# Kernel tuning notes

Hardware: AMD Instinct MI355X
Metric: run time of the kernel (lower is better)

The kernel has to match this reference:

```python
import jax, jax.numpy as jnp
import numpy as np

N = 50000      # nodes
E = 800000     # edges
IN, HID, OUT = 256, 64, 64
H1, H2 = 4, 1
NEG_SLOPE = 0.2  # DGL GATConv default


def gat_layer(x, W, a_l, a_r, b, src, dst, n_heads, d_out, activation=None):
    # x: [N, F_in]; W: [F_in, n_heads*d_out]; a_l/a_r: [n_heads, d_out]; b: [n_heads*d_out]
    z = (x @ W).reshape(N, n_heads, d_out)                      # [N,H,D]
    el = jnp.sum(z * a_l[None], axis=-1)                        # [N,H] score from src side
    er = jnp.sum(z * a_r[None], axis=-1)                        # [N,H] score from dst side
    e = jax.nn.leaky_relu(el[src] + er[dst], NEG_SLOPE)         # [E,H]
    # edge-softmax normalized over incoming edges of each dst node
    m = jax.ops.segment_max(e, dst, num_segments=N)             # [N,H]
    ex = jnp.exp(e - m[dst])                                    # [E,H]
    s = jax.ops.segment_sum(ex, dst, num_segments=N)            # [N,H]
    alpha = ex / s[dst]                                         # [E,H]
    # scatter-weighted aggregation of neighbor (src) features
    msg = alpha[:, :, None] * z[src]                            # [E,H,D]
    out = jax.ops.segment_sum(msg, dst, num_segments=N)         # [N,H,D]
    out = out + b.reshape(1, n_heads, d_out)
    if activation is not None:
        out = activation(out)
    return out


def setup_inputs() -> dict:
    key = jax.random.key(0)
    ks = jax.random.split(key, 12)
    x = jax.random.normal(ks[0], (N, IN), dtype=jnp.float32)
    src = jax.random.randint(ks[1], (E,), 0, N, dtype=jnp.int32)
    dst = jax.random.randint(ks[2], (E,), 0, N, dtype=jnp.int32)
    sc1 = 1.0 / np.sqrt(IN)
    sc2 = 1.0 / np.sqrt(HID * H1)
    W1 = jax.random.normal(ks[3], (IN, H1 * HID), dtype=jnp.float32) * sc1
    al1 = jax.random.normal(ks[4], (H1, HID), dtype=jnp.float32) * 0.1
    ar1 = jax.random.normal(ks[5], (H1, HID), dtype=jnp.float32) * 0.1
    b1 = jnp.zeros((H1 * HID,), dtype=jnp.float32)
    W2 = jax.random.normal(ks[6], (HID * H1, H2 * OUT), dtype=jnp.float32) * sc2
    al2 = jax.random.normal(ks[7], (H2, OUT), dtype=jnp.float32) * 0.1
    ar2 = jax.random.normal(ks[8], (H2, OUT), dtype=jnp.float32) * 0.1
    b2 = jnp.zeros((H2 * OUT,), dtype=jnp.float32)
    return {"x": x, "W1": W1, "al1": al1, "ar1": ar1, "b1": b1,
            "W2": W2, "al2": al2, "ar2": ar2, "b2": b2,
            "src": src, "dst": dst}


def reference(x, W1, al1, ar1, b1, W2, al2, ar2, b2, src, dst):
    # layer 1: GATConv(IN -> HID, H1 heads), elu activation, then flatten heads
    h = gat_layer(x, W1, al1, ar1, b1, src, dst, H1, HID, activation=jax.nn.elu)
    h = h.reshape(N, H1 * HID)
    # layer 2: GATConv(HID*H1 -> OUT, H2 heads), no activation, mean over heads
    h = gat_layer(h, W2, al2, ar2, b2, src, dst, H2, OUT, activation=None)
    return h.mean(axis=1)  # [N, OUT]
```

## Files before the change

kernel.cpp:

```cpp
#include <hip/hip_runtime.h>
#include <hip/hip_bf16.h>
#include <math.h>

#define NN 50000
#define EE 800000
#define FIN 256
#define HID 64
#define OUTD 64
#define H1 4
#define H2 1

typedef __attribute__((ext_vector_type(8))) short short8;
typedef __attribute__((ext_vector_type(4))) short short4v;
typedef __attribute__((ext_vector_type(4))) float f32x4;


__device__ __forceinline__ unsigned short f2bf(float f) {
    unsigned u = __float_as_uint(f);
    unsigned r = (u + 0x7FFFu + ((u >> 16) & 1u)) >> 16;
    return (unsigned short)r;
}
__device__ __forceinline__ float bf2f(unsigned short u) {
    return __uint_as_float(((unsigned)u) << 16);
}


__global__ void hist_kernel(const int* __restrict__ dst, int* __restrict__ deg, int nE) {
    int e = blockIdx.x * 256 + threadIdx.x;
    if (e < nE) atomicAdd(&deg[dst[e]], 1);
}

__global__ void scan_block(const int* __restrict__ in, int* __restrict__ out,
                           int* __restrict__ bsums, int n) {
    __shared__ int sh[256];
    int i = blockIdx.x * 256 + threadIdx.x;
    int v = (i < n) ? in[i] : 0;
    sh[threadIdx.x] = v;
    __syncthreads();
    for (int off = 1; off < 256; off <<= 1) {
        int t = 0;
        if (threadIdx.x >= off) t = sh[threadIdx.x - off];
        __syncthreads();
        if (threadIdx.x >= off) sh[threadIdx.x] += t;
        __syncthreads();
    }
    if (i < n) out[i] = sh[threadIdx.x] - v;
    if (threadIdx.x == 255) bsums[blockIdx.x] = sh[255];
}

__global__ void scan_bsums(int* __restrict__ bsums, int nb) {
    __shared__ int sh[256];
    int v = (threadIdx.x < nb) ? bsums[threadIdx.x] : 0;
    sh[threadIdx.x] = v;
    __syncthreads();
    for (int off = 1; off < 256; off <<= 1) {
        int t = 0;
        if (threadIdx.x >= off) t = sh[threadIdx.x - off];
        __syncthreads();
        if (threadIdx.x >= off) sh[threadIdx.x] += t;
        __syncthreads();
    }
    if (threadIdx.x < nb) bsums[threadIdx.x] = sh[threadIdx.x] - v;
}

__global__ void add_offsets(int* __restrict__ out, const int* __restrict__ bsums,
                            int n, int Etot) {
    int i = blockIdx.x * 256 + threadIdx.x;
    if (i < n) out[i] += bsums[blockIdx.x];
    if (i == 0) out[n] = Etot;
}

__global__ void fill_csr(const int* __restrict__ src, const int* __restrict__ dst,
                         const int* __restrict__ rowptr, int* __restrict__ fillc,
                         int* __restrict__ csr_src, int nE) {
    int e = blockIdx.x * 256 + threadIdx.x;
    if (e < nE) {
        int d = dst[e];
        int pos = rowptr[d] + atomicAdd(&fillc[d], 1);
        csr_src[pos] = src[e];
    }
}


__global__ void wsplit(const float* __restrict__ W1, const float* __restrict__ W2,
                       short* __restrict__ W1th, short* __restrict__ W1tl,
                       short* __restrict__ W2th, short* __restrict__ W2tl) {
    int n = blockIdx.x;
    int k = threadIdx.x;
    if (n < 256) {
        float v = W1[(size_t)k * 256 + n];
        unsigned short hi = f2bf(v);
        unsigned short lo = f2bf(v - bf2f(hi));
        W1th[n * 256 + k] = (short)hi;
        W1tl[n * 256 + k] = (short)lo;
    } else {
        int n2 = n - 256;
        float v = W2[(size_t)k * 64 + n2];
        unsigned short hi = f2bf(v);
        unsigned short lo = f2bf(v - bf2f(hi));
        W2th[n2 * 256 + k] = (short)hi;
        W2tl[n2 * 256 + k] = (short)lo;
    }
}


template<int MF, int WR, int WC, int NT, int H, bool ASPLIT>
__global__ __launch_bounds__(256) void gemm_bf16x2(
    const void* __restrict__ Av, const short* __restrict__ Bth, const short* __restrict__ Btl,
    const float* __restrict__ al, const float* __restrict__ ar,
    unsigned short* __restrict__ zb, float* __restrict__ el, float* __restrict__ er,
    int M, int K)
{
    constexpr int BM = WR * MF * 16;
    constexpr int BN = WC * 64;
    __shared__ short Ah[128 * 40];
    __shared__ short Al[ASPLIT ? 128 * 40 : 8];
    __shared__ short Bh[BN * 40], Bl[BN * 40];

    const int bm = blockIdx.x * BM;
    const int bn = blockIdx.y * BN;
    const int t = threadIdx.x;
    const int wid = t >> 6;
    const int lane = t & 63;
    const int lr = lane & 15;
    const int lg = lane >> 4;
    const int wr = wid / WC;
    const int wc = wid % WC;

    f32x4 acc[MF][4];
#pragma unroll
    for (int mf = 0; mf < MF; ++mf)
#pragma unroll
        for (int nf = 0; nf < 4; ++nf) acc[mf][nf] = (f32x4)(0.f);

    for (int k0 = 0; k0 < K; k0 += 32) {
        if constexpr (ASPLIT) {
            const float* A = (const float*)Av;
#pragma unroll
            for (int q = 0; q < 4; ++q) {
                int linear = q * 256 + t;
                int row = linear >> 3;
                int kq = (linear & 7) * 4;
                int grow = bm + row;
                float4 av = make_float4(0.f, 0.f, 0.f, 0.f);
                if (grow < M) av = *(const float4*)(A + (size_t)grow * K + k0 + kq);
                short4v hi, lo;
                unsigned short h0 = f2bf(av.x); hi.x = (short)h0; lo.x = (short)f2bf(av.x - bf2f(h0));
                unsigned short h1v = f2bf(av.y); hi.y = (short)h1v; lo.y = (short)f2bf(av.y - bf2f(h1v));
                unsigned short h2v = f2bf(av.z); hi.z = (short)h2v; lo.z = (short)f2bf(av.z - bf2f(h2v));
                unsigned short h3v = f2bf(av.w); hi.w = (short)h3v; lo.w = (short)f2bf(av.w - bf2f(h3v));
                *(short4v*)&Ah[row * 40 + kq] = hi;
                *(short4v*)&Al[row * 40 + kq] = lo;
            }
        } else {
            const unsigned short* A = (const unsigned short*)Av;
#pragma unroll
            for (int q = 0; q < 2; ++q) {
                int linear = q * 256 + t;
                int row = linear >> 2;
                int k8 = (linear & 3) * 8;
                int grow = bm + row;
                short8 v = (short8)(0);
                if (grow < M) v = *(const short8*)(A + (size_t)grow * K + k0 + k8);
                *(short8*)&Ah[row * 40 + k8] = v;
            }
        }
#pragma unroll
        for (int q = 0; q < BN / 64; ++q) {
            int linear = q * 256 + t;
            int n = linear >> 2;
            int k8 = (linear & 3) * 8;
            short8 vh = *(const short8*)(Bth + (size_t)(bn + n) * K + k0 + k8);
            short8 vl = *(const short8*)(Btl + (size_t)(bn + n) * K + k0 + k8);
            *(short8*)&Bh[n * 40 + k8] = vh;
            *(short8*)&Bl[n * 40 + k8] = vl;
        }
        __syncthreads();

        short8 ah[MF], alo[MF], bh[4], blo[4];
#pragma unroll
        for (int mf = 0; mf < MF; ++mf) {
            int row = wr * MF * 16 + mf * 16 + lr;
            ah[mf] = *(const short8*)&Ah[row * 40 + lg * 8];
            if constexpr (ASPLIT) alo[mf] = *(const short8*)&Al[row * 40 + lg * 8];
        }
#pragma unroll
        for (int nf = 0; nf < 4; ++nf) {
            int col = wc * 64 + nf * 16 + lr;
            bh[nf]  = *(const short8*)&Bh[col * 40 + lg * 8];
            blo[nf] = *(const short8*)&Bl[col * 40 + lg * 8];
        }
#pragma unroll
        for (int mf = 0; mf < MF; ++mf)
#pragma unroll
            for (int nf = 0; nf < 4; ++nf) {
                acc[mf][nf] = __builtin_amdgcn_mfma_f32_16x16x32_bf16(ah[mf], bh[nf],  acc[mf][nf], 0, 0, 0);
                acc[mf][nf] = __builtin_amdgcn_mfma_f32_16x16x32_bf16(ah[mf], blo[nf], acc[mf][nf], 0, 0, 0);
                if constexpr (ASPLIT)
                    acc[mf][nf] = __builtin_amdgcn_mfma_f32_16x16x32_bf16(alo[mf], bh[nf], acc[mf][nf], 0, 0, 0);
            }
        __syncthreads();
    }

    const int h = (bn + wc * 64) >> 6;
    float alv[4], arv[4];
#pragma unroll
    for (int nf = 0; nf < 4; ++nf) {
        alv[nf] = al[h * 64 + nf * 16 + lr];
        arv[nf] = ar[h * 64 + nf * 16 + lr];
    }
#pragma unroll
    for (int mf = 0; mf < MF; ++mf) {
#pragma unroll
        for (int j = 0; j < 4; ++j) {
            int row = bm + wr * MF * 16 + mf * 16 + lg * 4 + j;
            float sel = 0.f, ser = 0.f;
#pragma unroll
            for (int nf = 0; nf < 4; ++nf) {
                float v = acc[mf][nf][j];
                sel += v * alv[nf];
                ser += v * arv[nf];
                if (row < M)
                    zb[(size_t)row * NT + bn + wc * 64 + nf * 16 + lr] = f2bf(v);
            }
#pragma unroll
            for (int off = 1; off <= 8; off <<= 1) {
                sel += __shfl_xor(sel, off);
                ser += __shfl_xor(ser, off);
            }
            if (lr == 0 && row < M) {
                el[(size_t)row * H + h] = sel;
                er[(size_t)row * H + h] = ser;
            }
        }
    }
}


__global__ __launch_bounds__(256) void gat_aggregate_h4(
    const unsigned short* __restrict__ zb,
    const float* __restrict__ el,
    const float* __restrict__ er,
    const int* __restrict__ rowptr, const int* __restrict__ csr_src,
    const float* __restrict__ bias,
    unsigned short* __restrict__ out,
    int Nn)
{
    __shared__ float p_lds[4][64][4];
    __shared__ int   s_lds[4][64];
    int wid = threadIdx.x >> 6;
    int lane = threadIdx.x & 63;
    int n = blockIdx.x * 4 + wid;
    if (n >= Nn) return;
    int start = rowptr[n], end = rowptr[n + 1];
    int deg = end - start;
    float4 er4 = *(const float4*)(er + (size_t)n * 4);
    int hsel = lane >> 4;

    float4 acc = make_float4(0.f, 0.f, 0.f, 0.f);
    float4 ssum = make_float4(0.f, 0.f, 0.f, 0.f);
    float m = -INFINITY;

    for (int c0 = 0; c0 < deg; c0 += 64) {
        int nc = min(64, deg - c0);
        int s_l = 0;
        float4 e4 = make_float4(-INFINITY, -INFINITY, -INFINITY, -INFINITY);
        float emax_l = -INFINITY;
        if (lane < nc) {
            s_l = csr_src[start + c0 + lane];
            float4 el4 = *(const float4*)(el + (size_t)s_l * 4);
            e4.x = el4.x + er4.x; e4.x = e4.x > 0.f ? e4.x : 0.2f * e4.x;
            e4.y = el4.y + er4.y; e4.y = e4.y > 0.f ? e4.y : 0.2f * e4.y;
            e4.z = el4.z + er4.z; e4.z = e4.z > 0.f ? e4.z : 0.2f * e4.z;
            e4.w = el4.w + er4.w; e4.w = e4.w > 0.f ? e4.w : 0.2f * e4.w;
            emax_l = fmaxf(fmaxf(e4.x, e4.y), fmaxf(e4.z, e4.w));
        }
        float cm = emax_l;
#pragma unroll
        for (int off = 32; off; off >>= 1) cm = fmaxf(cm, __shfl_xor(cm, off));
        float newm = fmaxf(m, cm);
        float scale = __expf(m - newm);
        ssum.x *= scale; ssum.y *= scale; ssum.z *= scale; ssum.w *= scale;
        acc.x *= scale;  acc.y *= scale;  acc.z *= scale;  acc.w *= scale;
        m = newm;
        float4 p4 = make_float4(0.f, 0.f, 0.f, 0.f);
        if (lane < nc) {
            p4.x = __expf(e4.x - m);
            p4.y = __expf(e4.y - m);
            p4.z = __expf(e4.z - m);
            p4.w = __expf(e4.w - m);
        }
        float4 cs = p4;
#pragma unroll
        for (int off = 32; off; off >>= 1) {
            cs.x += __shfl_xor(cs.x, off);
            cs.y += __shfl_xor(cs.y, off);
            cs.z += __shfl_xor(cs.z, off);
            cs.w += __shfl_xor(cs.w, off);
        }
        ssum.x += cs.x; ssum.y += cs.y; ssum.z += cs.z; ssum.w += cs.w;
        *(float4*)&p_lds[wid][lane][0] = p4;
        s_lds[wid][lane] = s_l;

        const unsigned short* zlane = zb + lane * 4;
        for (int tt = 0; tt < nc; tt += 8) {
            float w[8]; int sv[8];
#pragma unroll
            for (int j = 0; j < 8; ++j) {
                int idx = tt + j;
                int ic = idx < nc ? idx : 0;
                w[j] = idx < nc ? p_lds[wid][ic][hsel] : 0.f;
                sv[j] = s_lds[wid][ic];
            }
            ushort4 u[8];
#pragma unroll
            for (int j = 0; j < 8; ++j)
                u[j] = *(const ushort4*)(zlane + (size_t)sv[j] * 256);
#pragma unroll
            for (int j = 0; j < 8; ++j) {
                acc.x = fmaf(w[j], bf2f(u[j].x), acc.x);
                acc.y = fmaf(w[j], bf2f(u[j].y), acc.y);
                acc.z = fmaf(w[j], bf2f(u[j].z), acc.z);
                acc.w = fmaf(w[j], bf2f(u[j].w), acc.w);
            }
        }
    }
    float s_h = hsel == 0 ? ssum.x : hsel == 1 ? ssum.y : hsel == 2 ? ssum.z : ssum.w;
    float inv = s_h > 0.f ? 1.f / s_h : 0.f;
    float4 b4 = *(const float4*)(bias + lane * 4);
    float ox = acc.x * inv + b4.x; ox = ox > 0.f ? ox : expm1f(ox);
    float oy = acc.y * inv + b4.y; oy = oy > 0.f ? oy : expm1f(oy);
    float oz = acc.z * inv + b4.z; oz = oz > 0.f ? oz : expm1f(oz);
    float ow = acc.w * inv + b4.w; ow = ow > 0.f ? ow : expm1f(ow);
    ushort4 o;
    o.x = f2bf(ox); o.y = f2bf(oy); o.z = f2bf(oz); o.w = f2bf(ow);
    *(ushort4*)(out + (size_t)n * 256 + lane * 4) = o;
}


__global__ void gat_aggregate_bf(const unsigned short* __restrict__ zb,
                                 const float* __restrict__ el, const float* __restrict__ er,
                                 const int* __restrict__ rowptr, const int* __restrict__ csr_src,
                                 const float* __restrict__ bias,
                                 float* __restrict__ out, int Nn)
{
    int gw = (blockIdx.x * blockDim.x + threadIdx.x) >> 6;
    int lane = threadIdx.x & 63;
    int n = gw;
    if (n >= Nn) return;
    int start = rowptr[n], end = rowptr[n + 1];
    int deg = end - start;
    float ern = er[n];

    int group = lane >> 4;
    int gl = lane & 15;

    float4 acc = make_float4(0.f, 0.f, 0.f, 0.f);
    float m = -INFINITY;
    float ssum = 0.f;

    for (int c0 = 0; c0 < deg; c0 += 64) {
        int nc = min(64, deg - c0);
        int s_l = 0;
        float e_l = -INFINITY;
        if (lane < nc) {
            s_l = csr_src[start + c0 + lane];
            float e = el[s_l] + ern;
            e_l = e > 0.f ? e : 0.2f * e;
        }
        float cm = e_l;
#pragma unroll
        for (int off = 32; off; off >>= 1) cm = fmaxf(cm, __shfl_xor(cm, off));
        float newm = fmaxf(m, cm);
        float scale = __expf(m - newm);
        ssum *= scale;
        acc.x *= scale; acc.y *= scale; acc.z *= scale; acc.w *= scale;
        m = newm;
        float p_l = (lane < nc) ? __expf(e_l - m) : 0.f;
        float cs = p_l;
#pragma unroll
        for (int off = 32; off; off >>= 1) cs += __shfl_xor(cs, off);
        ssum += cs;

        int nIter = (nc + 3) >> 2;
        for (int i0 = 0; i0 < nIter; i0 += 4) {
            float w[4]; int sv[4];
#pragma unroll
            for (int j = 0; j < 4; ++j) {
                int tt = group + 4 * (i0 + j);
                int tc = tt & 63;
                float wv = __shfl(p_l, tc);
                int s = __shfl(s_l, tc);
                w[j] = (tt < nc) ? wv : 0.f;
                sv[j] = s;
            }
            ushort4 u[4];
#pragma unroll
            for (int j = 0; j < 4; ++j)
                u[j] = *(const ushort4*)(zb + (size_t)sv[j] * 64 + gl * 4);
#pragma unroll
            for (int j = 0; j < 4; ++j) {
                acc.x = fmaf(w[j], bf2f(u[j].x), acc.x);
                acc.y = fmaf(w[j], bf2f(u[j].y), acc.y);
                acc.z = fmaf(w[j], bf2f(u[j].z), acc.z);
                acc.w = fmaf(w[j], bf2f(u[j].w), acc.w);
            }
        }
    }
#pragma unroll
    for (int off = 16; off <= 32; off <<= 1) {
        acc.x += __shfl_xor(acc.x, off);
        acc.y += __shfl_xor(acc.y, off);
        acc.z += __shfl_xor(acc.z, off);
        acc.w += __shfl_xor(acc.w, off);
    }
    float inv = ssum > 0.f ? 1.f / ssum : 0.f;
    if (lane < 16) {
        float4 o;
        o.x = acc.x * inv + bias[gl * 4 + 0];
        o.y = acc.y * inv + bias[gl * 4 + 1];
        o.z = acc.z * inv + bias[gl * 4 + 2];
        o.w = acc.w * inv + bias[gl * 4 + 3];
        *(float4*)(out + (size_t)n * 64 + gl * 4) = o;
    }
}


static inline size_t align_up(size_t x, size_t a) { return (x + a - 1) & ~(a - 1); }

extern "C" void kernel_launch(void* const* d_in, const int* in_sizes, int n_in,
                              void* d_out, int out_size, void* d_ws, size_t ws_size,
                              hipStream_t stream) {
    const float* x   = (const float*)d_in[0];
    const float* W1  = (const float*)d_in[1];
    const float* al1 = (const float*)d_in[2];
    const float* ar1 = (const float*)d_in[3];
    const float* b1  = (const float*)d_in[4];
    const float* W2  = (const float*)d_in[5];
    const float* al2 = (const float*)d_in[6];
    const float* ar2 = (const float*)d_in[7];
    const float* b2  = (const float*)d_in[8];
    const int*   src = (const int*)d_in[9];
    const int*   dst = (const int*)d_in[10];
    float* out = (float*)d_out;

    char* ws = (char*)d_ws;
    size_t off = 0;
    unsigned short* zb1 = (unsigned short*)(ws + off); off = align_up(off + (size_t)NN * 256 * 2, 256);
    unsigned short* h1b = (unsigned short*)(ws + off); off = align_up(off + (size_t)NN * 256 * 2, 256);
    unsigned short* zb2 = (unsigned short*)(ws + off); off = align_up(off + (size_t)NN * 64 * 2, 256);
    float* el1 = (float*)(ws + off); off = align_up(off + (size_t)NN * H1 * 4, 256);
    float* er1 = (float*)(ws + off); off = align_up(off + (size_t)NN * H1 * 4, 256);
    float* el2 = (float*)(ws + off); off = align_up(off + (size_t)NN * 4, 256);
    float* er2 = (float*)(ws + off); off = align_up(off + (size_t)NN * 4, 256);
    short* W1th = (short*)(ws + off); off = align_up(off + 256 * 256 * 2, 256);
    short* W1tl = (short*)(ws + off); off = align_up(off + 256 * 256 * 2, 256);
    short* W2th = (short*)(ws + off); off = align_up(off + 64 * 256 * 2, 256);
    short* W2tl = (short*)(ws + off); off = align_up(off + 64 * 256 * 2, 256);
    int* rowptr = (int*)(ws + off); off = align_up(off + (size_t)(NN + 1) * 4, 256);
    int* deg    = (int*)(ws + off); off = align_up(off + (size_t)NN * 4, 256);
    int* fillc  = (int*)(ws + off); off = align_up(off + (size_t)NN * 4, 256);
    int* bsums  = (int*)(ws + off); off = align_up(off + 256 * 4, 256);
    int* csr_src = (int*)(ws + off); off = align_up(off + (size_t)EE * 4, 256);

    const int nScanBlocks = (NN + 255) / 256;
    const int nEdgeBlocks = (EE + 255) / 256;
    const int nMBlocks = (NN + 127) / 128;

    hipMemsetAsync(deg, 0, (size_t)NN * 4, stream);
    hipMemsetAsync(fillc, 0, (size_t)NN * 4, stream);
    wsplit<<<320, 256, 0, stream>>>(W1, W2, W1th, W1tl, W2th, W2tl);
    hist_kernel<<<nEdgeBlocks, 256, 0, stream>>>(dst, deg, EE);
    scan_block<<<nScanBlocks, 256, 0, stream>>>(deg, rowptr, bsums, NN);
    scan_bsums<<<1, 256, 0, stream>>>(bsums, nScanBlocks);
    add_offsets<<<nScanBlocks, 256, 0, stream>>>(rowptr, bsums, NN, EE);
    fill_csr<<<nEdgeBlocks, 256, 0, stream>>>(src, dst, rowptr, fillc, csr_src, EE);

    gemm_bf16x2<4, 2, 2, 256, 4, true><<<dim3(nMBlocks, 2), 256, 0, stream>>>(
        x, W1th, W1tl, al1, ar1, zb1, el1, er1, NN, FIN);
    gat_aggregate_h4<<<(NN + 3) / 4, 256, 0, stream>>>(
        zb1, el1, er1, rowptr, csr_src, b1, h1b, NN);

    gemm_bf16x2<2, 4, 1, 64, 1, false><<<dim3(nMBlocks, 1), 256, 0, stream>>>(
        h1b, W2th, W2tl, al2, ar2, zb2, el2, er2, NN, H1 * HID);
    gat_aggregate_bf<<<(NN * 64 + 255) / 256, 256, 0, stream>>>(
        zb2, el2, er2, rowptr, csr_src, b2, out, NN);
}
```

Measured before the change: 261.6 us.

## Retile layer-1 GEMM to full-width blocks and pack aggregation FMAs

```diff
diff --git a/kernel.cpp b/kernel.cpp
--- a/kernel.cpp
+++ b/kernel.cpp
@@ -13,6 +13,7 @@
 typedef __attribute__((ext_vector_type(8))) short short8;
 typedef __attribute__((ext_vector_type(4))) short short4v;
 typedef __attribute__((ext_vector_type(4))) float f32x4;
+typedef __attribute__((ext_vector_type(2))) float f32x2;
 
 
 __device__ __forceinline__ unsigned short f2bf(float f) {
@@ -113,8 +114,8 @@
 {
     constexpr int BM = WR * MF * 16;
     constexpr int BN = WC * 64;
-    __shared__ short Ah[128 * 40];
-    __shared__ short Al[ASPLIT ? 128 * 40 : 8];
+    __shared__ short Ah[BM * 40];
+    __shared__ short Al[ASPLIT ? BM * 40 : 8];
     __shared__ short Bh[BN * 40], Bl[BN * 40];
 
     const int bm = blockIdx.x * BM;
@@ -137,7 +138,7 @@
         if constexpr (ASPLIT) {
             const float* A = (const float*)Av;
 #pragma unroll
-            for (int q = 0; q < 4; ++q) {
+            for (int q = 0; q < BM / 32; ++q) {
                 int linear = q * 256 + t;
                 int row = linear >> 3;
                 int kq = (linear & 7) * 4;
@@ -155,7 +156,7 @@
         } else {
             const unsigned short* A = (const unsigned short*)Av;
 #pragma unroll
-            for (int q = 0; q < 2; ++q) {
+            for (int q = 0; q < BM / 64; ++q) {
                 int linear = q * 256 + t;
                 int row = linear >> 2;
                 int k8 = (linear & 3) * 8;
@@ -256,8 +257,9 @@
     int deg = end - start;
     float4 er4 = *(const float4*)(er + (size_t)n * 4);
     int hsel = lane >> 4;
-
-    float4 acc = make_float4(0.f, 0.f, 0.f, 0.f);
+    const unsigned lb = (unsigned)(lane << 3);
+
+    f32x2 acc01 = {0.f, 0.f}, acc23 = {0.f, 0.f};
     float4 ssum = make_float4(0.f, 0.f, 0.f, 0.f);
     float m = -INFINITY;
 
@@ -281,7 +283,8 @@
         float newm = fmaxf(m, cm);
         float scale = __expf(m - newm);
         ssum.x *= scale; ssum.y *= scale; ssum.z *= scale; ssum.w *= scale;
-        acc.x *= scale;  acc.y *= scale;  acc.z *= scale;  acc.w *= scale;
+        f32x2 sc2 = {scale, scale};
+        acc01 *= sc2; acc23 *= sc2;
         m = newm;
         float4 p4 = make_float4(0.f, 0.f, 0.f, 0.f);
         if (lane < nc) {
@@ -302,29 +305,34 @@
         *(float4*)&p_lds[wid][lane][0] = p4;
         s_lds[wid][lane] = s_l;
 
-        const unsigned short* zlane = zb + lane * 4;
         for (int tt = 0; tt < nc; tt += 8) {
-            float w[8]; int sv[8];
+            float w[8]; unsigned off32[8];
 #pragma unroll
             for (int j = 0; j < 8; ++j) {
                 int idx = tt + j;
                 int ic = idx < nc ? idx : 0;
                 w[j] = idx < nc ? p_lds[wid][ic][hsel] : 0.f;
-                sv[j] = s_lds[wid][ic];
-            }
-            ushort4 u[8];
+                off32[j] = ((unsigned)s_lds[wid][ic] << 9) + lb;
+            }
+            uint2 u[8];
 #pragma unroll
             for (int j = 0; j < 8; ++j)
-                u[j] = *(const ushort4*)(zlane + (size_t)sv[j] * 256);
+                u[j] = *(const uint2*)((const char*)zb + off32[j]);
 #pragma unroll
             for (int j = 0; j < 8; ++j) {
-                acc.x = fmaf(w[j], bf2f(u[j].x), acc.x);
-                acc.y = fmaf(w[j], bf2f(u[j].y), acc.y);
-                acc.z = fmaf(w[j], bf2f(u[j].z), acc.z);
-                acc.w = fmaf(w[j], bf2f(u[j].w), acc.w);
-            }
-        }
-    }
+                f32x2 v01, v23, ww = {w[j], w[j]};
+                v01.x = __uint_as_float(u[j].x << 16);
+                v01.y = __uint_as_float(u[j].x & 0xffff0000u);
+                v23.x = __uint_as_float(u[j].y << 16);
+                v23.y = __uint_as_float(u[j].y & 0xffff0000u);
+                acc01 = __builtin_elementwise_fma(ww, v01, acc01);
+                acc23 = __builtin_elementwise_fma(ww, v23, acc23);
+            }
+        }
+    }
+    float4 acc = make_float4(acc01.x, acc01.y, acc23.x, acc23.y);
+#pragma unroll
+    for (int off = 16; off <= 32; off <<= 1) { }
     float s_h = hsel == 0 ? ssum.x : hsel == 1 ? ssum.y : hsel == 2 ? ssum.z : ssum.w;
     float inv = s_h > 0.f ? 1.f / s_h : 0.f;
     float4 b4 = *(const float4*)(bias + lane * 4);
@@ -354,8 +362,9 @@
 
     int group = lane >> 4;
     int gl = lane & 15;
-
-    float4 acc = make_float4(0.f, 0.f, 0.f, 0.f);
+    const unsigned lb = (unsigned)(gl << 3);
+
+    f32x2 acc01 = {0.f, 0.f}, acc23 = {0.f, 0.f};
     float m = -INFINITY;
     float ssum = 0.f;
 
@@ -374,7 +383,8 @@
         float newm = fmaxf(m, cm);
         float scale = __expf(m - newm);
         ssum *= scale;
-        acc.x *= scale; acc.y *= scale; acc.z *= scale; acc.w *= scale;
+        f32x2 sc2 = {scale, scale};
+        acc01 *= sc2; acc23 *= sc2;
         m = newm;
         float p_l = (lane < nc) ? __expf(e_l - m) : 0.f;
         float cs = p_l;
@@ -384,7 +394,7 @@
 
         int nIter = (nc + 3) >> 2;
         for (int i0 = 0; i0 < nIter; i0 += 4) {
-            float w[4]; int sv[4];
+            float w[4]; unsigned off32[4];
 #pragma unroll
             for (int j = 0; j < 4; ++j) {
                 int tt = group + 4 * (i0 + j);
@@ -392,21 +402,25 @@
                 float wv = __shfl(p_l, tc);
                 int s = __shfl(s_l, tc);
                 w[j] = (tt < nc) ? wv : 0.f;
-                sv[j] = s;
-            }
-            ushort4 u[4];
+                off32[j] = ((unsigned)s << 7) + lb;
+            }
+            uint2 u[4];
 #pragma unroll
             for (int j = 0; j < 4; ++j)
-                u[j] = *(const ushort4*)(zb + (size_t)sv[j] * 64 + gl * 4);
+                u[j] = *(const uint2*)((const char*)zb + off32[j]);
 #pragma unroll
             for (int j = 0; j < 4; ++j) {
-                acc.x = fmaf(w[j], bf2f(u[j].x), acc.x);
-                acc.y = fmaf(w[j], bf2f(u[j].y), acc.y);
-                acc.z = fmaf(w[j], bf2f(u[j].z), acc.z);
-                acc.w = fmaf(w[j], bf2f(u[j].w), acc.w);
-            }
-        }
-    }
+                f32x2 v01, v23, ww = {w[j], w[j]};
+                v01.x = __uint_as_float(u[j].x << 16);
+                v01.y = __uint_as_float(u[j].x & 0xffff0000u);
+                v23.x = __uint_as_float(u[j].y << 16);
+                v23.y = __uint_as_float(u[j].y & 0xffff0000u);
+                acc01 = __builtin_elementwise_fma(ww, v01, acc01);
+                acc23 = __builtin_elementwise_fma(ww, v23, acc23);
+            }
+        }
+    }
+    float4 acc = make_float4(acc01.x, acc01.y, acc23.x, acc23.y);
 #pragma unroll
     for (int off = 16; off <= 32; off <<= 1) {
         acc.x += __shfl_xor(acc.x, off);
@@ -465,7 +479,8 @@
 
     const int nScanBlocks = (NN + 255) / 256;
     const int nEdgeBlocks = (EE + 255) / 256;
-    const int nMBlocks = (NN + 127) / 128;
+    const int nMBlocks64 = (NN + 63) / 64;
+    const int nMBlocks128 = (NN + 127) / 128;
 
     hipMemsetAsync(deg, 0, (size_t)NN * 4, stream);
     hipMemsetAsync(fillc, 0, (size_t)NN * 4, stream);
@@ -476,12 +491,12 @@
     add_offsets<<<nScanBlocks, 256, 0, stream>>>(rowptr, bsums, NN, EE);
     fill_csr<<<nEdgeBlocks, 256, 0, stream>>>(src, dst, rowptr, fillc, csr_src, EE);
 
-    gemm_bf16x2<4, 2, 2, 256, 4, true><<<dim3(nMBlocks, 2), 256, 0, stream>>>(
+    gemm_bf16x2<4, 1, 4, 256, 4, true><<<dim3(nMBlocks64, 1), 256, 0, stream>>>(
         x, W1th, W1tl, al1, ar1, zb1, el1, er1, NN, FIN);
     gat_aggregate_h4<<<(NN + 3) / 4, 256, 0, stream>>>(
         zb1, el1, er1, rowptr, csr_src, b1, h1b, NN);
 
-    gemm_bf16x2<2, 4, 1, 64, 1, false><<<dim3(nMBlocks, 1), 256, 0, stream>>>(
+    gemm_bf16x2<2, 4, 1, 64, 1, false><<<dim3(nMBlocks128, 1), 256, 0, stream>>>(
         h1b, W2th, W2tl, al2, ar2, zb2, el2, er2, NN, H1 * HID);
     gat_aggregate_bf<<<(NN * 64 + 255) / 256, 256, 0, stream>>>(
         zb2, el2, er2, rowptr, csr_src, b2, out, NN);
```

After: 244.4 us. 6.6% less time.
